# Kernel optimization log

Hardware: AMD Instinct MI355X
Metric: run time of the kernel (lower is better)

The kernel has to match this reference:

```python
import jax, jax.numpy as jnp
import numpy as np

B, S, D, H = 4, 2048, 1024, 16
HD = D // H

def setup_inputs() -> dict:
    key = jax.random.key(0)
    ks = jax.random.split(key, 6)
    scale = 1.0 / np.sqrt(D)
    x = jax.random.normal(ks[0], (B, S, D), dtype=jnp.float32)
    q_w = jax.random.normal(ks[1], (D, D), dtype=jnp.float32) * scale
    k_w = jax.random.normal(ks[2], (D, D), dtype=jnp.float32) * scale
    v_w = jax.random.normal(ks[3], (D, D), dtype=jnp.float32) * scale
    o_w = jax.random.normal(ks[4], (D, D), dtype=jnp.float32) * scale
    zb = jnp.zeros((D,), dtype=jnp.float32)
    return {"x": x, "q_w": q_w, "q_b": zb, "k_w": k_w, "k_b": zb,
            "v_w": v_w, "v_b": zb, "o_w": o_w, "o_b": zb}

def reference(x, q_w, q_b, k_w, k_b, v_w, v_b, o_w, o_b):
    b, s, d = x.shape
    # projections; weights stored as (in, out) so y = x @ W + b
    q = (x @ q_w + q_b).reshape(b, s, H, HD).transpose(0, 2, 1, 3)  # [b,h,s,hd]
    k = (x @ k_w + k_b).reshape(b, s, H, HD).transpose(0, 2, 1, 3)
    v = (x @ v_w + v_b).reshape(b, s, H, HD).transpose(0, 2, 1, 3)
    attn = jnp.einsum('bhqd,bhkd->bhqk', q, k) * (HD ** -0.5)  # [b,h,s,s]
    attn = jax.nn.softmax(attn, axis=-1)
    out = jnp.einsum('bhqk,bhkd->bhqd', attn, v)  # [b,h,s,hd]
    out = out.transpose(0, 2, 1, 3).reshape(b, s, d)
    return out @ o_w + o_b
```

## Files before the change

kernel.cpp:

```cpp
#include <hip/hip_runtime.h>
#include <hip/hip_bf16.h>

typedef __bf16 bf16;
typedef __bf16 bf16x4 __attribute__((ext_vector_type(4)));
typedef __bf16 bf16x8 __attribute__((ext_vector_type(8)));
typedef float f32x4 __attribute__((ext_vector_type(4)));
typedef float f32x16 __attribute__((ext_vector_type(16)));

#define NB 4
#define SEQ 2048
#define DM 1024
#define NH 16
#define HDIM 64
#define MTOT (NB*SEQ)
#define BH_STRIDE (SEQ * HDIM)

#define QSCALE 0.18033688011112042f

#define ASYNC16(ldsp, gp) __builtin_amdgcn_global_load_lds( \
    (const __attribute__((address_space(1))) void*)(gp),    \
    (__attribute__((address_space(3))) void*)(ldsp), 16, 0, 0)

__global__ void cvt_x_kernel(const float* __restrict__ x, bf16* __restrict__ xb, int n4) {
  int i = blockIdx.x * blockDim.x + threadIdx.x;
  int stride = gridDim.x * blockDim.x;
  for (; i < n4; i += stride) {
    float4 v = ((const float4*)x)[i];
    bf16x4 o = {(bf16)v.x, (bf16)v.y, (bf16)v.z, (bf16)v.w};
    ((bf16x4*)xb)[i] = o;
  }
}

__global__ void cvt_w_kernel(const float* __restrict__ w0, const float* __restrict__ w1,
                             const float* __restrict__ w2, const float* __restrict__ w3,
                             bf16* __restrict__ wt) {
  __shared__ float t[32][33];
  const float* w = blockIdx.z == 0 ? w0 : blockIdx.z == 1 ? w1 : blockIdx.z == 2 ? w2 : w3;
  bf16* o = wt + (size_t)blockIdx.z * DM * DM;
  int n0 = blockIdx.x * 32, k0 = blockIdx.y * 32;
  int tx = threadIdx.x, ty = threadIdx.y;
  #pragma unroll
  for (int i = 0; i < 4; i++) t[ty + 8*i][tx] = w[(size_t)(k0 + ty + 8*i) * DM + n0 + tx];
  __syncthreads();
  #pragma unroll
  for (int i = 0; i < 4; i++) o[(size_t)(n0 + ty + 8*i) * DM + k0 + tx] = (bf16)t[tx][ty + 8*i];
}

template<int EPI>
__global__ __launch_bounds__(256) void gemm128(
    const bf16* __restrict__ A, const bf16* __restrict__ Bt,
    const float* __restrict__ bq, const float* __restrict__ bk, const float* __restrict__ bv,
    bf16* __restrict__ oq, bf16* __restrict__ ok, bf16* __restrict__ ovt,
    float* __restrict__ of) {
  const int tid = threadIdx.x;
  const int lane = tid & 63;
  const int wid = tid >> 6;
  const int wr = wid >> 1, wc = wid & 1;
  const int bm = blockIdx.y * 128;
  const int bn = blockIdx.x * 128;

  __shared__ __align__(16) bf16 As[2][128 * 32];
  __shared__ __align__(16) bf16 Bs[2][128 * 32];

  f32x4 acc[4][4] = {};

  const bf16* ga = A  + (size_t)(bm + (tid >> 2)) * DM + (tid & 3) * 8;
  const bf16* gb = Bt + (size_t)(bn + (tid >> 2)) * DM + (tid & 3) * 8;

  ASYNC16(&As[0][tid * 8], ga);
  ASYNC16(&As[0][2048 + tid * 8], ga + 64 * DM);
  ASYNC16(&Bs[0][tid * 8], gb);
  ASYNC16(&Bs[0][2048 + tid * 8], gb + 64 * DM);

  const int r0 = lane & 15;
  const int kc = (lane >> 4) * 8;

  for (int kt = 0; kt < DM / 32; ++kt) {
    const int cur = kt & 1;
    __syncthreads();
    if (kt + 1 < DM / 32) {
      const int nk = (kt + 1) * 32;
      ASYNC16(&As[cur ^ 1][tid * 8], ga + nk);
      ASYNC16(&As[cur ^ 1][2048 + tid * 8], ga + 64 * DM + nk);
      ASYNC16(&Bs[cur ^ 1][tid * 8], gb + nk);
      ASYNC16(&Bs[cur ^ 1][2048 + tid * 8], gb + 64 * DM + nk);
    }
    bf16x8 af[4], bfr[4];
    #pragma unroll
    for (int i = 0; i < 4; i++) {
      af[i]  = *(const bf16x8*)&As[cur][(wr * 64 + i * 16 + r0) * 32 + kc];
      bfr[i] = *(const bf16x8*)&Bs[cur][(wc * 64 + i * 16 + r0) * 32 + kc];
    }
    #pragma unroll
    for (int i = 0; i < 4; i++)
      #pragma unroll
      for (int j = 0; j < 4; j++)
        acc[i][j] = __builtin_amdgcn_mfma_f32_16x16x32_bf16(af[i], bfr[j], acc[i][j], 0, 0, 0);
  }

  if (EPI == 0) {
    const int which = bn >> 10;
    const float* bp = which == 0 ? bq : which == 1 ? bk : bv;
    const float scale = (which == 0) ? QSCALE : 1.0f;
    #pragma unroll
    for (int j = 0; j < 4; j++) {
      const int n = bn + wc * 64 + j * 16 + r0;
      const int dcol = n & 1023;
      const int h = dcol >> 6, hd = dcol & 63;
      const float bias = bp[dcol];
      const int qk_d = (hd >> 4) * 512 + ((hd >> 3) & 1) * 256 + (hd & 7);
      const int v_d  = (hd >> 5) * 2048 + (hd & 31) * 8;
      #pragma unroll
      for (int i = 0; i < 4; i++)
        #pragma unroll
        for (int r = 0; r < 4; r++) {
          const int m = bm + wr * 64 + i * 16 + (lane >> 4) * 4 + r;
          const int b_ = m >> 11, s_ = m & 2047;
          const float v = (acc[i][j][r] + bias) * scale;
          if (which <= 1) {
            const size_t off = (size_t)(b_ * NH + h) * BH_STRIDE
                             + (s_ >> 5) * 2048 + (s_ & 31) * 8 + qk_d;
            (which == 0 ? oq : ok)[off] = (bf16)v;
          } else {
            const size_t off = (size_t)(b_ * NH + h) * BH_STRIDE
                             + (s_ >> 6) * 4096 + ((s_ >> 4) & 3) * 512
                             + ((s_ >> 3) & 1) * 256 + (s_ & 7) + v_d;
            ovt[off] = (bf16)v;
          }
        }
    }
  } else {
    #pragma unroll
    for (int j = 0; j < 4; j++) {
      const int n = bn + wc * 64 + j * 16 + r0;
      const float bias = bq[n];
      #pragma unroll
      for (int i = 0; i < 4; i++)
        #pragma unroll
        for (int r = 0; r < 4; r++) {
          const int m = bm + wr * 64 + i * 16 + (lane >> 4) * 4 + r;
          of[(size_t)m * DM + n] = acc[i][j][r] + bias;
        }
    }
  }
}

__global__ __launch_bounds__(256) void attn_kernel(
    const bf16* __restrict__ Q, const bf16* __restrict__ Kf, const bf16* __restrict__ Vf,
    bf16* __restrict__ O) {
  const int tid = threadIdx.x;
  const int lane = tid & 63;
  const int wid = tid >> 6;
  const int hi = lane >> 5;
  const int q5 = lane & 31;
  const int qt = blockIdx.x;
  const int h = blockIdx.y;
  const int b = blockIdx.z;

  const bf16* qp = Q  + (size_t)(b * NH + h) * BH_STRIDE + qt * 8192;
  const bf16* kp = Kf + (size_t)(b * NH + h) * BH_STRIDE;
  const bf16* vp = Vf + (size_t)(b * NH + h) * BH_STRIDE;

  __shared__ __align__(16) bf16 KsF[8192];
  __shared__ __align__(16) bf16 VsF[8192];
  __shared__ __align__(16) bf16 Pp[4][32 * 68];

  ASYNC16(&KsF[tid * 8], qp + tid * 8);
  ASYNC16(&KsF[2048 + tid * 8], qp + 2048 + tid * 8);
  ASYNC16(&KsF[4096 + tid * 8], qp + 4096 + tid * 8);
  ASYNC16(&KsF[6144 + tid * 8], qp + 6144 + tid * 8);
  __syncthreads();
  bf16x8 qf[4];
  #pragma unroll
  for (int ks = 0; ks < 4; ks++)
    qf[ks] = *(const bf16x8*)&KsF[wid * 2048 + ks * 512 + hi * 256 + q5 * 8];
  __syncthreads();

  ASYNC16(&KsF[tid * 8], kp + tid * 8);
  ASYNC16(&KsF[2048 + tid * 8], kp + 2048 + tid * 8);
  ASYNC16(&VsF[tid * 8], vp + tid * 8);
  ASYNC16(&VsF[2048 + tid * 8], vp + 2048 + tid * 8);
  __syncthreads();

  float m_run = -1e30f, l_run = 0.f;
  f32x16 oaccA = {}, oaccB = {};

  bf16* pwb = &Pp[wid][q5 * 68 + hi * 4];
  const bf16* prd = &Pp[wid][q5 * 68 + hi * 8];

  for (int kt = 0; kt < SEQ / 64; ++kt) {
    const int curo = (kt & 1) * 4096;
    if (kt + 1 < SEQ / 64) {
      const int nxo = curo ^ 4096;
      const bf16* gk = kp + (size_t)(kt + 1) * 4096;
      ASYNC16(&KsF[nxo + tid * 8], gk + tid * 8);
      ASYNC16(&KsF[nxo + 2048 + tid * 8], gk + 2048 + tid * 8);
      const bf16* gv = vp + (size_t)(kt + 1) * 4096;
      ASYNC16(&VsF[nxo + tid * 8], gv + tid * 8);
      ASYNC16(&VsF[nxo + 2048 + tid * 8], gv + 2048 + tid * 8);
    }

    f32x16 sc0 = {}, sc1 = {};
    __builtin_amdgcn_s_setprio(1);
    #pragma unroll
    for (int ks = 0; ks < 4; ks++) {
      const bf16x8 kf0 = *(const bf16x8*)&KsF[curo + ks * 512 + hi * 256 + q5 * 8];
      sc0 = __builtin_amdgcn_mfma_f32_32x32x16_bf16(kf0, qf[ks], sc0, 0, 0, 0);
      const bf16x8 kf1 = *(const bf16x8*)&KsF[curo + 2048 + ks * 512 + hi * 256 + q5 * 8];
      sc1 = __builtin_amdgcn_mfma_f32_32x32x16_bf16(kf1, qf[ks], sc1, 0, 0, 0);
    }
    __builtin_amdgcn_s_setprio(0);

    float pmax = sc0[0];
    #pragma unroll
    for (int r = 1; r < 16; r++) pmax = fmaxf(pmax, sc0[r]);
    #pragma unroll
    for (int r = 0; r < 16; r++) pmax = fmaxf(pmax, sc1[r]);
    pmax = fmaxf(pmax, __shfl_xor(pmax, 32));

    if (__any(pmax > m_run + 8.f)) {
      const float mnew = fmaxf(m_run, pmax);
      const float fac = exp2f(m_run - mnew);
      l_run *= fac;
      #pragma unroll
      for (int r = 0; r < 16; r++) { oaccA[r] *= fac; oaccB[r] *= fac; }
      m_run = mnew;
    }

    float psum = 0.f;
    #pragma unroll
    for (int rg = 0; rg < 4; rg++) {
      bf16x4 pk0, pk1;
      #pragma unroll
      for (int e = 0; e < 4; e++) {
        const float pv0 = exp2f(sc0[rg * 4 + e] - m_run);
        psum += pv0;
        pk0[e] = (bf16)pv0;
        const float pv1 = exp2f(sc1[rg * 4 + e] - m_run);
        psum += pv1;
        pk1[e] = (bf16)pv1;
      }
      *(bf16x4*)(pwb + rg * 8) = pk0;
      *(bf16x4*)(pwb + 32 + rg * 8) = pk1;
    }
    psum += __shfl_xor(psum, 32);
    l_run += psum;

    __builtin_amdgcn_s_setprio(1);
    #pragma unroll
    for (int kvs = 0; kvs < 4; kvs++) {
      const bf16x8 pf = *(const bf16x8*)(prd + kvs * 16);
      const bf16x8 vf0 = *(const bf16x8*)&VsF[curo + kvs * 512 + hi * 256 + q5 * 8];
      oaccA = __builtin_amdgcn_mfma_f32_32x32x16_bf16(vf0, pf, oaccA, 0, 0, 0);
      const bf16x8 vf1 = *(const bf16x8*)&VsF[curo + 2048 + kvs * 512 + hi * 256 + q5 * 8];
      oaccB = __builtin_amdgcn_mfma_f32_32x32x16_bf16(vf1, pf, oaccB, 0, 0, 0);
    }
    __builtin_amdgcn_s_setprio(0);
    __syncthreads();
  }

  const float inv = 1.0f / l_run;
  const int qrow = qt * 128 + wid * 32 + q5;
  bf16* ob = (bf16*)&O[((size_t)b * SEQ + qrow) * DM + h * HDIM + hi * 4];
  #pragma unroll
  for (int rg = 0; rg < 4; rg++) {
    bf16x4 ovA, ovB;
    #pragma unroll
    for (int e = 0; e < 4; e++) {
      ovA[e] = (bf16)(oaccA[rg * 4 + e] * inv);
      ovB[e] = (bf16)(oaccB[rg * 4 + e] * inv);
    }
    *(bf16x4*)(ob + rg * 8) = ovA;
    *(bf16x4*)(ob + 32 + rg * 8) = ovB;
  }
}

extern "C" void kernel_launch(void* const* d_in, const int* in_sizes, int n_in,
                              void* d_out, int out_size, void* d_ws, size_t ws_size,
                              hipStream_t stream) {
  (void)in_sizes; (void)n_in; (void)out_size; (void)ws_size;
  const float* x   = (const float*)d_in[0];
  const float* q_w = (const float*)d_in[1];
  const float* q_b = (const float*)d_in[2];
  const float* k_w = (const float*)d_in[3];
  const float* k_b = (const float*)d_in[4];
  const float* v_w = (const float*)d_in[5];
  const float* v_b = (const float*)d_in[6];
  const float* o_w = (const float*)d_in[7];
  const float* o_b = (const float*)d_in[8];
  float* out = (float*)d_out;

  char* p = (char*)d_ws;
  bf16* xb = (bf16*)p;  p += (size_t)MTOT * DM * 2;
  bf16* wt = (bf16*)p;  p += (size_t)4 * DM * DM * 2;
  bf16* qq = (bf16*)p;  p += (size_t)MTOT * DM * 2;
  bf16* kk = (bf16*)p;  p += (size_t)MTOT * DM * 2;
  bf16* vt = (bf16*)p;  p += (size_t)MTOT * DM * 2;

  cvt_x_kernel<<<1024, 256, 0, stream>>>(x, xb, MTOT * DM / 4);
  cvt_w_kernel<<<dim3(32, 32, 4), dim3(32, 8), 0, stream>>>(q_w, k_w, v_w, o_w, wt);

  gemm128<0><<<dim3(24, 64), 256, 0, stream>>>(xb, wt, q_b, k_b, v_b, qq, kk, vt, nullptr);

  attn_kernel<<<dim3(SEQ / 128, NH, NB), 256, 0, stream>>>(qq, kk, vt, xb);

  gemm128<1><<<dim3(8, 64), 256, 0, stream>>>(xb, wt + (size_t)3 * DM * DM, o_b, nullptr, nullptr,
                                              nullptr, nullptr, nullptr, out);
}
```

Before: 379.5 us.

## Remap workgroups for XCD locality and pass P through registers via lane shuffles

After: 344.0 us. 9.3% less time.

```diff
diff --git a/kernel.cpp b/kernel.cpp
--- a/kernel.cpp
+++ b/kernel.cpp
@@ -2,6 +2,7 @@
 #include <hip/hip_bf16.h>
 
 typedef __bf16 bf16;
+typedef __bf16 bf16x2 __attribute__((ext_vector_type(2)));
 typedef __bf16 bf16x4 __attribute__((ext_vector_type(4)));
 typedef __bf16 bf16x8 __attribute__((ext_vector_type(8)));
 typedef float f32x4 __attribute__((ext_vector_type(4)));
@@ -46,7 +47,7 @@
   for (int i = 0; i < 4; i++) o[(size_t)(n0 + ty + 8*i) * DM + k0 + tx] = (bf16)t[tx][ty + 8*i];
 }
 
-template<int EPI>
+template<int EPI, int NX>
 __global__ __launch_bounds__(256) void gemm128(
     const bf16* __restrict__ A, const bf16* __restrict__ Bt,
     const float* __restrict__ bq, const float* __restrict__ bk, const float* __restrict__ bv,
@@ -56,8 +57,10 @@
   const int lane = tid & 63;
   const int wid = tid >> 6;
   const int wr = wid >> 1, wc = wid & 1;
-  const int bm = blockIdx.y * 128;
-  const int bn = blockIdx.x * 128;
+  const int nwg = NX * 64;
+  const int wg = (blockIdx.x & 7) * (nwg >> 3) + (blockIdx.x >> 3);
+  const int bm = (wg / NX) * 128;
+  const int bn = (wg % NX) * 128;
 
   __shared__ __align__(16) bf16 As[2][128 * 32];
   __shared__ __align__(16) bf16 Bs[2][128 * 32];
@@ -153,9 +156,10 @@
   const int wid = tid >> 6;
   const int hi = lane >> 5;
   const int q5 = lane & 31;
-  const int qt = blockIdx.x;
-  const int h = blockIdx.y;
-  const int b = blockIdx.z;
+  const int wg = (blockIdx.x & 7) * 128 + (blockIdx.x >> 3);
+  const int qt = wg & 15;
+  const int h = (wg >> 4) & 15;
+  const int b = wg >> 8;
 
   const bf16* qp = Q  + (size_t)(b * NH + h) * BH_STRIDE + qt * 8192;
   const bf16* kp = Kf + (size_t)(b * NH + h) * BH_STRIDE;
@@ -163,7 +167,6 @@
 
   __shared__ __align__(16) bf16 KsF[8192];
   __shared__ __align__(16) bf16 VsF[8192];
-  __shared__ __align__(16) bf16 Pp[4][32 * 68];
 
   ASYNC16(&KsF[tid * 8], qp + tid * 8);
   ASYNC16(&KsF[2048 + tid * 8], qp + 2048 + tid * 8);
@@ -185,9 +188,6 @@
   float m_run = -1e30f, l_run = 0.f;
   f32x16 oaccA = {}, oaccB = {};
 
-  bf16* pwb = &Pp[wid][q5 * 68 + hi * 4];
-  const bf16* prd = &Pp[wid][q5 * 68 + hi * 8];
-
   for (int kt = 0; kt < SEQ / 64; ++kt) {
     const int curo = (kt & 1) * 4096;
     if (kt + 1 < SEQ / 64) {
@@ -227,33 +227,49 @@
       m_run = mnew;
     }
 
+    int Pa[2][4], Pb[2][4];
     float psum = 0.f;
     #pragma unroll
-    for (int rg = 0; rg < 4; rg++) {
-      bf16x4 pk0, pk1;
-      #pragma unroll
-      for (int e = 0; e < 4; e++) {
-        const float pv0 = exp2f(sc0[rg * 4 + e] - m_run);
-        psum += pv0;
-        pk0[e] = (bf16)pv0;
-        const float pv1 = exp2f(sc1[rg * 4 + e] - m_run);
-        psum += pv1;
-        pk1[e] = (bf16)pv1;
+    for (int t = 0; t < 2; t++) {
+      #pragma unroll
+      for (int rg = 0; rg < 4; rg++) {
+        const float p0 = exp2f((t ? sc1 : sc0)[rg * 4 + 0] - m_run);
+        const float p1 = exp2f((t ? sc1 : sc0)[rg * 4 + 1] - m_run);
+        const float p2 = exp2f((t ? sc1 : sc0)[rg * 4 + 2] - m_run);
+        const float p3 = exp2f((t ? sc1 : sc0)[rg * 4 + 3] - m_run);
+        psum += (p0 + p1) + (p2 + p3);
+        union { bf16x2 v; int u; } a, bb;
+        a.v  = bf16x2{(bf16)p0, (bf16)p1};
+        bb.v = bf16x2{(bf16)p2, (bf16)p3};
+        Pa[t][rg] = a.u;
+        Pb[t][rg] = bb.u;
       }
-      *(bf16x4*)(pwb + rg * 8) = pk0;
-      *(bf16x4*)(pwb + 32 + rg * 8) = pk1;
     }
     psum += __shfl_xor(psum, 32);
     l_run += psum;
 
     __builtin_amdgcn_s_setprio(1);
     #pragma unroll
-    for (int kvs = 0; kvs < 4; kvs++) {
-      const bf16x8 pf = *(const bf16x8*)(prd + kvs * 16);
-      const bf16x8 vf0 = *(const bf16x8*)&VsF[curo + kvs * 512 + hi * 256 + q5 * 8];
-      oaccA = __builtin_amdgcn_mfma_f32_32x32x16_bf16(vf0, pf, oaccA, 0, 0, 0);
-      const bf16x8 vf1 = *(const bf16x8*)&VsF[curo + 2048 + kvs * 512 + hi * 256 + q5 * 8];
-      oaccB = __builtin_amdgcn_mfma_f32_32x32x16_bf16(vf1, pf, oaccB, 0, 0, 0);
+    for (int t = 0; t < 2; t++) {
+      #pragma unroll
+      for (int k1 = 0; k1 < 2; k1++) {
+        const int srcA  = hi ? Pa[t][2 * k1]     : Pa[t][2 * k1 + 1];
+        const int srcB  = hi ? Pb[t][2 * k1]     : Pb[t][2 * k1 + 1];
+        const int selfA = hi ? Pa[t][2 * k1 + 1] : Pa[t][2 * k1];
+        const int selfB = hi ? Pb[t][2 * k1 + 1] : Pb[t][2 * k1];
+        const int pulA = __shfl_xor(srcA, 32);
+        const int pulB = __shfl_xor(srcB, 32);
+        union { int4 i; bf16x8 v; } pf;
+        pf.i.x = hi ? pulA : selfA;
+        pf.i.y = hi ? pulB : selfB;
+        pf.i.z = hi ? selfA : pulA;
+        pf.i.w = hi ? selfB : pulB;
+        const int kvs = t * 2 + k1;
+        const bf16x8 vf0 = *(const bf16x8*)&VsF[curo + kvs * 512 + hi * 256 + q5 * 8];
+        oaccA = __builtin_amdgcn_mfma_f32_32x32x16_bf16(vf0, pf.v, oaccA, 0, 0, 0);
+        const bf16x8 vf1 = *(const bf16x8*)&VsF[curo + 2048 + kvs * 512 + hi * 256 + q5 * 8];
+        oaccB = __builtin_amdgcn_mfma_f32_32x32x16_bf16(vf1, pf.v, oaccB, 0, 0, 0);
+      }
     }
     __builtin_amdgcn_s_setprio(0);
     __syncthreads();
@@ -300,10 +316,10 @@
   cvt_x_kernel<<<1024, 256, 0, stream>>>(x, xb, MTOT * DM / 4);
   cvt_w_kernel<<<dim3(32, 32, 4), dim3(32, 8), 0, stream>>>(q_w, k_w, v_w, o_w, wt);
 
-  gemm128<0><<<dim3(24, 64), 256, 0, stream>>>(xb, wt, q_b, k_b, v_b, qq, kk, vt, nullptr);
-
-  attn_kernel<<<dim3(SEQ / 128, NH, NB), 256, 0, stream>>>(qq, kk, vt, xb);
-
-  gemm128<1><<<dim3(8, 64), 256, 0, stream>>>(xb, wt + (size_t)3 * DM * DM, o_b, nullptr, nullptr,
-                                              nullptr, nullptr, nullptr, out);
-}
+  gemm128<0, 24><<<1536, 256, 0, stream>>>(xb, wt, q_b, k_b, v_b, qq, kk, vt, nullptr);
+
+  attn_kernel<<<1024, 256, 0, stream>>>(qq, kk, vt, xb);
+
+  gemm128<1, 8><<<512, 256, 0, stream>>>(xb, wt + (size_t)3 * DM * DM, o_b, nullptr, nullptr,
+                                         nullptr, nullptr, nullptr, out);
+}
```
